# Kernel optimization log

Hardware: AMD Instinct MI355X
Metric: run time of the kernel (lower is better)

The kernel has to match this reference:

```python
import jax, jax.numpy as jnp
import numpy as np

EPS = 1e-6  # torch.nn.PairwiseDistance default eps (added to the difference)


def setup_inputs() -> dict:
    key = jax.random.key(0)
    k1, k2 = jax.random.split(key)
    support = jax.random.normal(k1, (25, 2560), dtype=jnp.float32)
    query = jax.random.normal(k2, (4096, 2560), dtype=jnp.float32)
    return {"support": support, "query": query, "n_way": 5, "k_shot": 5}


def reference(support, query, n_way, k_shot):
    # support: [n_way*k_shot, cdd], query: [qsize, cdd]
    qsize = query.shape[0]
    support = support.reshape(support.shape[0], -1)
    query = query.reshape(qsize, -1)
    # pairwise L2 distance with torch PairwiseDistance semantics: ||x1 - x2 + eps||_2
    diff = support[None, :, :] - query[:, None, :] + EPS  # [qsize, n_way*k_shot, cdd]
    dist = jnp.sqrt(jnp.sum(diff * diff, axis=-1))        # [qsize, n_way*k_shot]
    score = -dist.reshape(qsize, n_way, k_shot).sum(axis=2)  # [qsize, n_way]
    return score
```

## Files before the change

kernel.cpp:

```cpp
#include <hip/hip_runtime.h>
#include <hip/hip_bf16.h>
#include <math.h>


#define EPS 1e-6f
#define D 2560
#define NSUP 25
#define NQ 4096
#define NWAY 5
#define KSHOT 5

#define QR 4
#define BT 256
#define KITER 5
#define NSL 13
#define NACC 60
#define PH 30
#define STRIDE 31

__global__ void prep_kernel(const float* __restrict__ sup, float* __restrict__ ns) {
    const int s = blockIdx.x;
    const int t = threadIdx.x;
    float p = 0.f;
    #pragma unroll
    for (int k = 0; k < 10; ++k) {
        float v = sup[s * D + t + 256 * k] + EPS;
        p += v * v;
    }
    __shared__ float red[256];
    red[t] = p;
    __syncthreads();
    for (int off = 128; off > 0; off >>= 1) {
        if (t < off) red[t] += red[t + off];
        __syncthreads();
    }
    if (t == 0) ns[s] = red[0];
}

__global__ __launch_bounds__(BT, 2)
void pairwise_kernel(const float* __restrict__ q, const float* __restrict__ sup,
                     const float* __restrict__ ns, float* __restrict__ out) {
    const int t = threadIdx.x;
    const int lane = t & 63;
    const int wave = t >> 6;
    const int sg = wave >> 1;
    const int dg = wave & 1;
    const int row0 = blockIdx.x * QR;
    const int sup_base = sg * (NSL - 1);

    float acc[NACC];
    #pragma unroll
    for (int i = 0; i < NACC; ++i) acc[i] = 0.f;

    #pragma unroll 1
    for (int j = 0; j < KITER; ++j) {
        const int idx = 4 * lane + 512 * j + 256 * dg;
        float4 q4[QR];
        #pragma unroll
        for (int r = 0; r < QR; ++r)
            q4[r] = *reinterpret_cast<const float4*>(&q[(row0 + r) * D + idx]);
        #pragma unroll
        for (int r = 0; r < QR; ++r) {
            acc[52 + r] += (q4[r].x + q4[r].y) + (q4[r].z + q4[r].w);
            acc[56 + r] += q4[r].x * q4[r].x + q4[r].y * q4[r].y
                         + q4[r].z * q4[r].z + q4[r].w * q4[r].w;
        }
        #pragma unroll
        for (int g = 0; g < NSL; g += 4) {
            const int ge = (g + 4 < NSL) ? g + 4 : NSL;
            float4 a4[4];
            #pragma unroll
            for (int jj = g; jj < ge; ++jj)
                a4[jj - g] = *reinterpret_cast<const float4*>(&sup[(sup_base + jj) * D + idx]);
            #pragma unroll
            for (int jj = g; jj < ge; ++jj) {
                #pragma unroll
                for (int r = 0; r < QR; ++r) {
                    acc[r * NSL + jj] += a4[jj - g].x * q4[r].x + a4[jj - g].y * q4[r].y
                                       + a4[jj - g].z * q4[r].z + a4[jj - g].w * q4[r].w;
                }
            }
        }
    }

    __shared__ float buf[BT * STRIDE];
    __shared__ float red0[NACC];
    __shared__ float red1[NACC];
    __shared__ float dist[100];

    #pragma unroll
    for (int p = 0; p < 2; ++p) {
        #pragma unroll
        for (int v = 0; v < PH; ++v) buf[t * STRIDE + v] = acc[p * PH + v];
        __syncthreads();
        if ((wave == 0 || wave == 2) && lane < PH) {
            const int base = (wave >> 1) * 128;
            float s0 = 0.f, s1 = 0.f, s2 = 0.f, s3 = 0.f;
            for (int i = 0; i < 128; i += 4) {
                s0 += buf[(base + i + 0) * STRIDE + lane];
                s1 += buf[(base + i + 1) * STRIDE + lane];
                s2 += buf[(base + i + 2) * STRIDE + lane];
                s3 += buf[(base + i + 3) * STRIDE + lane];
            }
            const float tot = (s0 + s1) + (s2 + s3);
            if (wave == 0) red0[p * PH + lane] = tot;
            else           red1[p * PH + lane] = tot;
        }
        __syncthreads();
    }

    if (t < 100) {
        const int r = t / NSUP, s = t % NSUP;
        const float dot = (s < NSL) ? red0[r * NSL + s] : red1[r * NSL + (s - (NSL - 1))];
        const float d2 = ns[s] + red0[56 + r] - 2.f * (dot + EPS * red0[52 + r]);
        dist[t] = sqrtf(fmaxf(d2, 0.f));
    }
    __syncthreads();
    if (t < QR * NWAY) {
        const int r = t / NWAY, w = t % NWAY;
        float sc = 0.f;
        #pragma unroll
        for (int j = 0; j < KSHOT; ++j) sc += dist[r * NSUP + w * KSHOT + j];
        out[(row0 + r) * NWAY + w] = -sc;
    }
}

extern "C" void kernel_launch(void* const* d_in, const int* in_sizes, int n_in,
                              void* d_out, int out_size, void* d_ws, size_t ws_size,
                              hipStream_t stream) {
    const float* support = (const float*)d_in[0];
    const float* query   = (const float*)d_in[1];
    float* out = (float*)d_out;
    float* ns  = (float*)d_ws;

    prep_kernel<<<NSUP, 256, 0, stream>>>(support, ns);
    pairwise_kernel<<<NQ / QR, BT, 0, stream>>>(query, support, ns, out);
}
```

Baseline: 101.7 us.

## Stage query tiles in LDS via async global-to-LDS loads with double buffering

Query rows are now fetched by only half the waves using global_load_lds directly into a double-buffered LDS region. All waves then read them from LDS, and the next chunk is prefetched while the current chunk is computed. The LDS reduction buffer is reused for staging. This aims to remove duplicate global loads of the query and to overlap fetch with compute. In exchange it adds a block barrier every iteration, and it relies on async loads being complete at the barrier.

```diff
diff --git a/kernel.cpp b/kernel.cpp
--- a/kernel.cpp
+++ b/kernel.cpp
@@ -17,6 +17,13 @@
 #define NACC 60
 #define PH 30
 #define STRIDE 31
+
+__device__ __forceinline__ void async_q16(const float* gp, float* lp) {
+    __builtin_amdgcn_global_load_lds(
+        (const __attribute__((address_space(1))) void*)gp,
+        (__attribute__((address_space(3))) void*)lp,
+        16, 0, 0);
+}
 
 __global__ void prep_kernel(const float* __restrict__ sup, float* __restrict__ ns) {
     const int s = blockIdx.x;
@@ -48,23 +55,40 @@
     const int row0 = blockIdx.x * QR;
     const int sup_base = sg * (NSL - 1);
 
+    __shared__ float smem[BT * STRIDE];
+    __shared__ float red0[NACC];
+    __shared__ float red1[NACC];
+    __shared__ float dist[100];
+
+    if (sg == 0) {
+        #pragma unroll
+        for (int r = 0; r < QR; ++r)
+            async_q16(&q[(row0 + r) * D + 256 * dg + 4 * lane],
+                      &smem[dg * 1024 + r * 256]);
+    }
+    __syncthreads();
+
     float acc[NACC];
     #pragma unroll
     for (int i = 0; i < NACC; ++i) acc[i] = 0.f;
 
     #pragma unroll 1
     for (int j = 0; j < KITER; ++j) {
+        const int cur = j & 1, nxt = cur ^ 1;
         const int idx = 4 * lane + 512 * j + 256 * dg;
-        float4 q4[QR];
+
+        float4 qv[QR];
         #pragma unroll
         for (int r = 0; r < QR; ++r)
-            q4[r] = *reinterpret_cast<const float4*>(&q[(row0 + r) * D + idx]);
+            qv[r] = *reinterpret_cast<const float4*>(
+                        &smem[(cur * 2 + dg) * 1024 + r * 256 + 4 * lane]);
         #pragma unroll
         for (int r = 0; r < QR; ++r) {
-            acc[52 + r] += (q4[r].x + q4[r].y) + (q4[r].z + q4[r].w);
-            acc[56 + r] += q4[r].x * q4[r].x + q4[r].y * q4[r].y
-                         + q4[r].z * q4[r].z + q4[r].w * q4[r].w;
+            acc[52 + r] += (qv[r].x + qv[r].y) + (qv[r].z + qv[r].w);
+            acc[56 + r] += qv[r].x * qv[r].x + qv[r].y * qv[r].y
+                         + qv[r].z * qv[r].z + qv[r].w * qv[r].w;
         }
+
         #pragma unroll
         for (int g = 0; g < NSL; g += 4) {
             const int ge = (g + 4 < NSL) ? g + 4 : NSL;
@@ -76,31 +100,34 @@
             for (int jj = g; jj < ge; ++jj) {
                 #pragma unroll
                 for (int r = 0; r < QR; ++r) {
-                    acc[r * NSL + jj] += a4[jj - g].x * q4[r].x + a4[jj - g].y * q4[r].y
-                                       + a4[jj - g].z * q4[r].z + a4[jj - g].w * q4[r].w;
+                    acc[r * NSL + jj] += a4[jj - g].x * qv[r].x + a4[jj - g].y * qv[r].y
+                                       + a4[jj - g].z * qv[r].z + a4[jj - g].w * qv[r].w;
                 }
             }
         }
+
+        if (j < KITER - 1 && sg == 0) {
+            #pragma unroll
+            for (int r = 0; r < QR; ++r)
+                async_q16(&q[(row0 + r) * D + 512 * (j + 1) + 256 * dg + 4 * lane],
+                          &smem[(nxt * 2 + dg) * 1024 + r * 256]);
+        }
+        __syncthreads();
     }
-
-    __shared__ float buf[BT * STRIDE];
-    __shared__ float red0[NACC];
-    __shared__ float red1[NACC];
-    __shared__ float dist[100];
 
     #pragma unroll
     for (int p = 0; p < 2; ++p) {
         #pragma unroll
-        for (int v = 0; v < PH; ++v) buf[t * STRIDE + v] = acc[p * PH + v];
+        for (int v = 0; v < PH; ++v) smem[t * STRIDE + v] = acc[p * PH + v];
         __syncthreads();
         if ((wave == 0 || wave == 2) && lane < PH) {
             const int base = (wave >> 1) * 128;
             float s0 = 0.f, s1 = 0.f, s2 = 0.f, s3 = 0.f;
             for (int i = 0; i < 128; i += 4) {
-                s0 += buf[(base + i + 0) * STRIDE + lane];
-                s1 += buf[(base + i + 1) * STRIDE + lane];
-                s2 += buf[(base + i + 2) * STRIDE + lane];
-                s3 += buf[(base + i + 3) * STRIDE + lane];
+                s0 += smem[(base + i + 0) * STRIDE + lane];
+                s1 += smem[(base + i + 1) * STRIDE + lane];
+                s2 += smem[(base + i + 2) * STRIDE + lane];
+                s3 += smem[(base + i + 3) * STRIDE + lane];
             }
             const float tot = (s0 + s1) + (s2 + s3);
             if (wave == 0) red0[p * PH + lane] = tot;
```

Result: no change. 103.5 us (+1.7%).
